# Kernel optimization log

Measured on AMD Instinct MI355X. Metric: run time of the kernel, lower is better.

Reference implementation:

```python
import jax, jax.numpy as jnp
import numpy as np

B, T, C = 2, 2048, 1024
H = 16
D = C // H  # head_size = 64
FF = 4 * C
EPS = 1e-5


def _layernorm(x, g, b):
    mu = jnp.mean(x, axis=-1, keepdims=True)
    var = jnp.var(x, axis=-1, keepdims=True)
    return (x - mu) * jax.lax.rsqrt(var + EPS) * g + b


def setup_inputs() -> dict:
    key = jax.random.key(0)
    ks = jax.random.split(key, 12)
    s_in = 1.0 / np.sqrt(C)
    s_ff = 1.0 / np.sqrt(FF)
    return {
        "x": jax.random.normal(ks[0], (B, T, C), jnp.float32),
        "Wq": jax.random.uniform(ks[1], (H, C, D), jnp.float32, -s_in, s_in),
        "Wk": jax.random.uniform(ks[2], (H, C, D), jnp.float32, -s_in, s_in),
        "Wv": jax.random.uniform(ks[3], (H, C, D), jnp.float32, -s_in, s_in),
        "Wo": jax.random.uniform(ks[4], (C, C), jnp.float32, -s_in, s_in),
        "bo": jax.random.uniform(ks[5], (C,), jnp.float32, -s_in, s_in),
        "W1": jax.random.uniform(ks[6], (C, FF), jnp.float32, -s_in, s_in),
        "b1": jax.random.uniform(ks[7], (FF,), jnp.float32, -s_in, s_in),
        "W2": jax.random.uniform(ks[8], (FF, C), jnp.float32, -s_ff, s_ff),
        "b2": jax.random.uniform(ks[9], (C,), jnp.float32, -s_ff, s_ff),
        "g1": jnp.ones((C,), jnp.float32),
        "be1": jnp.zeros((C,), jnp.float32),
        "g2": jnp.ones((C,), jnp.float32),
        "be2": jnp.zeros((C,), jnp.float32),
    }


def reference(x, Wq, Wk, Wv, Wo, bo, W1, b1, W2, b2, g1, be1, g2, be2):
    h = _layernorm(x, g1, be1)
    # per-head projections (no bias), vectorized over heads
    q = jnp.einsum("btc,hcd->bhtd", h, Wq)
    k = jnp.einsum("btc,hcd->bhtd", h, Wk)
    v = jnp.einsum("btc,hcd->bhtd", h, Wv)
    # NOTE: original scales by n_embd**-0.5 (C, not head_size) -- faithful
    scores = jnp.einsum("bhtd,bhsd->bhts", q, k) * (C ** -0.5)
    causal = jnp.tril(jnp.ones((T, T), bool))
    scores = jnp.where(causal, scores, -jnp.inf)
    att = jax.nn.softmax(scores, axis=-1)
    out = jnp.einsum("bhts,bhsd->bhtd", att, v)
    out = out.transpose(0, 2, 1, 3).reshape(B, T, C)  # concat heads
    x = out @ Wo + bo + x  # attn residual (dropout=0 -> identity)
    h2 = _layernorm(x, g2, be2)
    ff = jax.nn.relu(h2 @ W1 + b1) @ W2 + b2
    return x + ff
```

## Files before the change

### kernel.cpp

```cpp
#include <hip/hip_runtime.h>
#include <stdint.h>

typedef unsigned short ushort_t;
typedef __attribute__((ext_vector_type(8))) short bf16x8;
typedef __attribute__((ext_vector_type(4))) float f32x4;

__device__ __forceinline__ unsigned short f2b(float f) {
  unsigned u = __float_as_uint(f);
  u += 0x7fffu + ((u >> 16) & 1u);
  return (unsigned short)(u >> 16);
}

__device__ __forceinline__ void async16(const void* g, void* l) {
  __builtin_amdgcn_global_load_lds(
      (const __attribute__((address_space(1))) void*)g,
      (__attribute__((address_space(3))) void*)l, 16, 0, 0);
}

__global__ __launch_bounds__(256) void ln_kernel(
    const float* __restrict__ x, const float* __restrict__ g,
    const float* __restrict__ be, ushort_t* __restrict__ out) {
  const int C = 1024;
  int row = blockIdx.x;
  const float4* xr = (const float4*)(x + (size_t)row * C);
  int tid = threadIdx.x;
  float4 v = xr[tid];
  float s = v.x + v.y + v.z + v.w;
  float sq = v.x * v.x + v.y * v.y + v.z * v.z + v.w * v.w;
  #pragma unroll
  for (int off = 32; off > 0; off >>= 1) {
    s += __shfl_xor(s, off);
    sq += __shfl_xor(sq, off);
  }
  __shared__ float ss[4], ssq[4];
  int wv = tid >> 6;
  if ((tid & 63) == 0) { ss[wv] = s; ssq[wv] = sq; }
  __syncthreads();
  s = ss[0] + ss[1] + ss[2] + ss[3];
  sq = ssq[0] + ssq[1] + ssq[2] + ssq[3];
  float mu = s * (1.f / C);
  float var = sq * (1.f / C) - mu * mu;
  float rs = rsqrtf(var + 1e-5f);
  float4 gv = ((const float4*)g)[tid];
  float4 bv = ((const float4*)be)[tid];
  ushort4 o;
  o.x = f2b((v.x - mu) * rs * gv.x + bv.x);
  o.y = f2b((v.y - mu) * rs * gv.y + bv.y);
  o.z = f2b((v.z - mu) * rs * gv.z + bv.z);
  o.w = f2b((v.w - mu) * rs * gv.w + bv.w);
  ((ushort4*)(out + (size_t)row * C))[tid] = o;
}

__global__ __launch_bounds__(256) void reduce2_kernel(
    const float* __restrict__ p0, const float* __restrict__ p1,
    const float* __restrict__ bias, const float* __restrict__ resid,
    float* __restrict__ out) {
  int idx = blockIdx.x * 256 + threadIdx.x;
  float4 a = ((const float4*)p0)[idx];
  float4 b = ((const float4*)p1)[idx];
  float4 r = ((const float4*)resid)[idx];
  float4 bi = ((const float4*)bias)[idx & 255];
  float4 o;
  o.x = a.x + b.x + r.x + bi.x;
  o.y = a.y + b.y + r.y + bi.y;
  o.z = a.z + b.z + r.z + bi.z;
  o.w = a.w + b.w + r.w + bi.w;
  ((float4*)out)[idx] = o;
}

__global__ __launch_bounds__(256) void transpose_all_kernel(
    const float* __restrict__ Wq, const float* __restrict__ Wk,
    const float* __restrict__ Wv, const float* __restrict__ Wo,
    const float* __restrict__ W1, const float* __restrict__ W2,
    ushort_t* __restrict__ qkvt, ushort_t* __restrict__ wot,
    ushort_t* __restrict__ w1t, ushort_t* __restrict__ w2t) {
  int bid = blockIdx.x;
  const float* in;
  ushort_t* out;
  int R, Cin, bx, by;
  if (bid < 3072) {
    int z = bid >> 6, rem = bid & 63;
    bx = rem & 1; by = rem >> 1;
    int wsel = z >> 4, h = z & 15;
    in = (wsel == 0 ? Wq : wsel == 1 ? Wk : Wv) + (size_t)h * 1024 * 64;
    out = qkvt + (size_t)wsel * 1024 * 1024 + (size_t)h * 1024 * 64;
    R = 1024; Cin = 64;
  } else if (bid < 4096) {
    int rem = bid - 3072;
    bx = rem & 31; by = rem >> 5;
    in = Wo; out = wot; R = 1024; Cin = 1024;
  } else if (bid < 8192) {
    int rem = bid - 4096;
    bx = rem & 127; by = rem >> 7;
    in = W1; out = w1t; R = 1024; Cin = 4096;
  } else {
    int rem = bid - 8192;
    bx = rem & 31; by = rem >> 5;
    in = W2; out = w2t; R = 4096; Cin = 1024;
  }
  __shared__ float tile[32][33];
  int c0 = bx * 32, r0 = by * 32;
  int tx = threadIdx.x, ty = threadIdx.y;
  #pragma unroll
  for (int i = 0; i < 4; i++)
    tile[ty + 8 * i][tx] = in[(size_t)(r0 + ty + 8 * i) * Cin + c0 + tx];
  __syncthreads();
  #pragma unroll
  for (int i = 0; i < 4; i++)
    out[(size_t)(c0 + ty + 8 * i) * R + r0 + tx] = f2b(tile[tx][ty + 8 * i]);
}

__global__ __launch_bounds__(256) void transpose_v_kernel(
    const ushort_t* __restrict__ qkv, ushort_t* __restrict__ vt) {
  __shared__ ushort_t tile[32][33];
  int bh = blockIdx.z;
  int b = bh >> 4, h = bh & 15;
  int d0 = blockIdx.x * 32, t0 = blockIdx.y * 32;
  int tx = threadIdx.x, ty = threadIdx.y;
  #pragma unroll
  for (int i = 0; i < 4; i++)
    tile[ty + 8 * i][tx] =
        qkv[(size_t)(b * 2048 + t0 + ty + 8 * i) * 3072 + 2048 + h * 64 + d0 + tx];
  __syncthreads();
  #pragma unroll
  for (int i = 0; i < 4; i++)
    vt[(size_t)(bh * 64 + d0 + ty + 8 * i) * 2048 + t0 + tx] = tile[tx][ty + 8 * i];
}

#define RD_A(DB, MB) \
  _Pragma("unroll") \
  for (int mf_ = 0; mf_ < 4; mf_++) { \
    af[(MB) + mf_][0] = *(const bf16x8*)&Als[DB][wm][(aRow + ((MB) + mf_) * 16) * 64 + rof0]; \
    af[(MB) + mf_][1] = *(const bf16x8*)&Als[DB][wm][(aRow + ((MB) + mf_) * 16) * 64 + rof1]; \
  }
#define RD_B(DB, NB) \
  _Pragma("unroll") \
  for (int nf_ = 0; nf_ < 2; nf_++) { \
    bf[(NB) + nf_][0] = *(const bf16x8*)&Bls[DB][bh][(bRow + ((NB) + nf_) * 16) * 64 + rof0]; \
    bf[(NB) + nf_][1] = *(const bf16x8*)&Bls[DB][bh][(bRow + ((NB) + nf_) * 16) * 64 + rof1]; \
  }
#define MMPH(MB, NB) \
  __builtin_amdgcn_s_barrier(); \
  asm volatile("s_waitcnt lgkmcnt(0)" ::: "memory"); \
  __builtin_amdgcn_sched_barrier(0); \
  __builtin_amdgcn_s_setprio(1); \
  _Pragma("unroll") \
  for (int mf_ = 0; mf_ < 4; mf_++) \
    _Pragma("unroll") \
    for (int nf_ = 0; nf_ < 2; nf_++) { \
      acc[(MB) + mf_][(NB) + nf_] = __builtin_amdgcn_mfma_f32_16x16x32_bf16( \
          af[(MB) + mf_][0], bf[(NB) + nf_][0], acc[(MB) + mf_][(NB) + nf_], 0, 0, 0); \
      acc[(MB) + mf_][(NB) + nf_] = __builtin_amdgcn_mfma_f32_16x16x32_bf16( \
          af[(MB) + mf_][1], bf[(NB) + nf_][1], acc[(MB) + mf_][(NB) + nf_], 0, 0, 0); \
    } \
  __builtin_amdgcn_s_setprio(0);
#define ENDPH __builtin_amdgcn_s_barrier();

template <int N, int K, int FLAGS>
__global__ __launch_bounds__(512, 2) void gemm256p8_kernel(
    const ushort_t* __restrict__ A, const ushort_t* __restrict__ Bt,
    const float* __restrict__ bias, void* __restrict__ outv) {
  constexpr int NBN = N / 256;
  constexpr int NT2 = K / 128;
  __shared__ __align__(16) ushort_t Als[2][2][128 * 64];
  __shared__ __align__(16) ushort_t Bls[2][2][128 * 64];
  int tid = threadIdx.x, w = tid >> 6, lane = tid & 63;
  int quad = lane >> 4, l16 = lane & 15;
  int wm = w >> 2, wn = w & 3;
  int bid = blockIdx.x;
  int bm = bid / NBN, bn = bid % NBN;
  int bm0 = bm * 256, bn0 = bn * 256;
  int lrow = (w << 3) + (lane >> 3);
  int kc8 = ((lane & 7) ^ ((lane >> 3) & 7)) << 3;
  const ushort_t* Ab = A + (size_t)(bm0 + lrow) * K + kc8;
  const ushort_t* Bb = Bt + (size_t)(bn0 + lrow) * K + kc8;
  int rof0 = (quad ^ (l16 & 7)) << 3;
  int rof1 = ((4 + quad) ^ (l16 & 7)) << 3;
  int bh = wn >> 1;
  int aRow = l16;
  int bRow = (wn & 1) * 64 + l16;

  auto stA = [&](int kt, int half, int db) {
    const ushort_t* g = Ab + (size_t)(half * 128) * K + kt * 64;
    ushort_t* l = &Als[db][half][w * 512];
    async16(g, l);
    async16(g + (size_t)64 * K, l + 4096);
  };
  auto stB = [&](int kt, int half, int db) {
    const ushort_t* g = Bb + (size_t)(half * 128) * K + kt * 64;
    ushort_t* l = &Bls[db][half][w * 512];
    async16(g, l);
    async16(g + (size_t)64 * K, l + 4096);
  };

  f32x4 acc[8][4];
  #pragma unroll
  for (int mf = 0; mf < 8; mf++)
    #pragma unroll
    for (int nf = 0; nf < 4; nf++) acc[mf][nf] = f32x4{0.f, 0.f, 0.f, 0.f};
  bf16x8 af[8][2], bf[4][2];

  stA(0, 0, 0); stA(0, 1, 0);
  stB(0, 0, 0); stB(0, 1, 0);
  stA(1, 0, 1); stA(1, 1, 1);
  asm volatile("s_waitcnt vmcnt(4)" ::: "memory");
  __builtin_amdgcn_s_barrier();

  #pragma unroll 1
  for (int i = 0; i < NT2; ++i) {
    bool lastI = (i == NT2 - 1);
    int t1 = 2 * i + 1;
    RD_A(0, 0)
    RD_B(0, 0)
    stB(t1, 0, 1);
    MMPH(0, 0)
    ENDPH
    RD_A(0, 4)
    stB(t1, 1, 1);
    MMPH(4, 0)
    ENDPH
    RD_B(0, 2)
    if (!lastI) stA(t1 + 1, 0, 0);
    MMPH(4, 2)
    ENDPH
    if (!lastI) stA(t1 + 1, 1, 0);
    MMPH(0, 2)
    if (!lastI) asm volatile("s_waitcnt vmcnt(4)" ::: "memory");
    else        asm volatile("s_waitcnt vmcnt(0)" ::: "memory");
    ENDPH
    RD_A(1, 0)
    RD_B(1, 0)
    if (!lastI) stB(t1 + 1, 0, 0);
    MMPH(0, 0)
    ENDPH
    RD_A(1, 4)
    if (!lastI) stB(t1 + 1, 1, 0);
    MMPH(4, 0)
    ENDPH
    RD_B(1, 2)
    if (!lastI) stA(t1 + 2, 0, 1);
    MMPH(4, 2)
    ENDPH
    if (!lastI) stA(t1 + 2, 1, 1);
    MMPH(0, 2)
    if (!lastI) asm volatile("s_waitcnt vmcnt(4)" ::: "memory");
    ENDPH
  }
  #pragma unroll
  for (int mf = 0; mf < 8; mf++)
    #pragma unroll
    for (int nf = 0; nf < 4; nf++)
      #pragma unroll
      for (int r = 0; r < 4; r++) {
        int row = bm0 + wm * 128 + mf * 16 + quad * 4 + r;
        int col = bn0 + wn * 64 + nf * 16 + l16;
        float v = acc[mf][nf][r];
        if constexpr (FLAGS & 4) v += bias[col];
        if constexpr (FLAGS & 1) v = fmaxf(v, 0.f);
        if constexpr ((FLAGS & 2) != 0)
          ((ushort_t*)outv)[(size_t)row * N + col] = f2b(v);
        else
          ((float*)outv)[(size_t)row * N + col] = v;
      }
}
#undef RD_A
#undef RD_B
#undef MMPH
#undef ENDPH

template <int N, int K, int FLAGS, int SK>
__global__ __launch_bounds__(256, 3) void gemm_bt64_kernel(
    const ushort_t* __restrict__ A, const ushort_t* __restrict__ Bt,
    const float* __restrict__ bias, const float* __restrict__ resid,
    void* __restrict__ outv, float* __restrict__ pp0, float* __restrict__ pp1) {
  constexpr int KS = K / SK;
  constexpr int NBM = 32;
  constexpr int NBN = N / 64;
  constexpr int NWG = NBM * NBN * SK;
  __shared__ ushort_t Als[2][128 * 32];
  __shared__ ushort_t Bls[2][64 * 32];
  int tid = threadIdx.x, w = tid >> 6, lane = tid & 63, quad = lane >> 4, l16 = lane & 15;
  int bid = blockIdx.x;
  int swz = (bid & 7) * (NWG / 8) + (bid >> 3);
  int z = 0;
  if constexpr (SK > 1) { z = swz / (NBM * NBN); swz -= z * (NBM * NBN); }
  int bm = swz / NBN, bn = swz - bm * NBN;
  int bm0 = bm * 128, bn0 = bn * 64;
  int koff = z * KS;
  int wm = (w >> 1) * 64, wn = (w & 1) * 32;
  f32x4 acc[4][2];
  #pragma unroll
  for (int i = 0; i < 4; i++)
    #pragma unroll
    for (int j = 0; j < 2; j++) acc[i][j] = f32x4{0.f, 0.f, 0.f, 0.f};
  const ushort_t* Ag = A + (size_t)bm0 * K + koff;
  const ushort_t* Bg = Bt + (size_t)bn0 * K + koff;
  int lr = lane >> 2, lco = (lane & 3) * 8;
  auto stage = [&](int k0, int bi) {
    async16(Ag + (size_t)(w * 32 + lr) * K + k0 + lco, &Als[bi][w * 1024]);
    async16(Ag + (size_t)(w * 32 + 16 + lr) * K + k0 + lco, &Als[bi][w * 1024 + 512]);
    async16(Bg + (size_t)(w * 16 + lr) * K + k0 + lco, &Bls[bi][w * 512]);
  };
  stage(0, 0);
  int s = 0;
  for (int k0 = 0; k0 < KS; k0 += 32, s ^= 1) {
    __syncthreads();
    if (k0 + 32 < KS) stage(k0 + 32, s ^ 1);
    bf16x8 af[4], bf[2];
    #pragma unroll
    for (int i = 0; i < 4; i++)
      af[i] = *(const bf16x8*)&Als[s][(wm + i * 16 + l16) * 32 + quad * 8];
    #pragma unroll
    for (int j = 0; j < 2; j++)
      bf[j] = *(const bf16x8*)&Bls[s][(wn + j * 16 + l16) * 32 + quad * 8];
    #pragma unroll
    for (int i = 0; i < 4; i++)
      #pragma unroll
      for (int j = 0; j < 2; j++)
        acc[i][j] = __builtin_amdgcn_mfma_f32_16x16x32_bf16(af[i], bf[j], acc[i][j], 0, 0, 0);
  }
  float* pdst = nullptr;
  if constexpr (SK > 1) pdst = z ? pp1 : pp0;
  #pragma unroll
  for (int i = 0; i < 4; i++)
    #pragma unroll
    for (int j = 0; j < 2; j++)
      #pragma unroll
      for (int r = 0; r < 4; r++) {
        int row = bm0 + wm + i * 16 + quad * 4 + r;
        int col = bn0 + wn + j * 16 + l16;
        float v = acc[i][j][r];
        if constexpr (SK > 1) {
          pdst[(size_t)row * N + col] = v;
        } else {
          if constexpr (FLAGS & 4) v += bias[col];
          if constexpr (FLAGS & 8) v += resid[(size_t)row * N + col];
          if constexpr (FLAGS & 1) v = fmaxf(v, 0.f);
          if constexpr ((FLAGS & 2) != 0)
            ((ushort_t*)outv)[(size_t)row * N + col] = f2b(v);
          else
            ((float*)outv)[(size_t)row * N + col] = v;
        }
      }
}

__global__ __launch_bounds__(256, 4) void attn_kernel(
    const ushort_t* __restrict__ qkv, const ushort_t* __restrict__ vt,
    ushort_t* __restrict__ out) {
  const int T = 2048, CC = 3072;
  __shared__ ushort_t Kls[2][2 * 64 * 32];
  __shared__ ushort_t Vls[2][2 * 64 * 32];
  int fid = blockIdx.x;
  int bh = (fid & 7) * 4 + ((fid >> 3) & 3);
  int qb = 31 - (fid >> 5);
  int b = bh >> 4, h = bh & 15;
  int q0 = qb * 64;
  int tid = threadIdx.x, w = tid >> 6, lane = tid & 63, quad = lane >> 4, l16 = lane & 15;
  int srow = w * 16 + (lane >> 2);
  int sco = (lane & 3) * 8;
  const ushort_t* kg = qkv + (size_t)(b * T + srow) * CC + 1024 + h * 64 + sco;
  const ushort_t* vg = vt + (size_t)(bh * 64 + srow) * T + sco;
  int q0s = q0 + w * 16;
  int trow = q0s + l16;
  const ushort_t* qp = qkv + (size_t)(b * T + trow) * CC + h * 64 + quad * 8;
  bf16x8 aq[2] = { *(const bf16x8*)qp, *(const bf16x8*)(qp + 32) };
  f32x4 O[4];
  #pragma unroll
  for (int i = 0; i < 4; i++) O[i] = f32x4{0.f, 0.f, 0.f, 0.f};
  float mrun = -1e30f, lrun = 0.f;
  const float ksc = 0.03125f * 1.44269504f;
  int src0 = (quad & 1) * 32 + l16;
  int src1 = src0 + 16;
  bool hiq = quad >= 2;
  auto stage = [&](int kb, int bi) {
    int s0 = kb * 64;
    async16(kg + (size_t)s0 * CC, &Kls[bi][w * 512]);
    async16(kg + (size_t)s0 * CC + 32, &Kls[bi][2048 + w * 512]);
    async16(vg + s0, &Vls[bi][w * 512]);
    async16(vg + s0 + 32, &Vls[bi][2048 + w * 512]);
  };
  stage(0, 0);
  for (int kb = 0; kb <= qb; kb++) {
    __syncthreads();
    if (kb < qb) stage(kb + 1, (kb + 1) & 1);
    int bi = kb & 1;
    int s0 = kb * 64;
    bf16x8 kfr[4][2], vfr[4][2];
    #pragma unroll
    for (int t = 0; t < 4; t++)
      #pragma unroll
      for (int ks = 0; ks < 2; ks++) {
        kfr[t][ks] = *(const bf16x8*)&Kls[bi][(ks * 64 + t * 16 + l16) * 32 + quad * 8];
        vfr[t][ks] = *(const bf16x8*)&Vls[bi][(ks * 64 + t * 16 + l16) * 32 + quad * 8];
      }
    f32x4 st[4];
    #pragma unroll
    for (int t = 0; t < 4; t++) {
      st[t] = f32x4{0.f, 0.f, 0.f, 0.f};
      #pragma unroll
      for (int ks = 0; ks < 2; ks++)
        st[t] = __builtin_amdgcn_mfma_f32_16x16x32_bf16(kfr[t][ks], aq[ks], st[t], 0, 0, 0);
    }
    float sv[4][4];
    float vmax = -1e30f;
    if (kb == qb) {
      #pragma unroll
      for (int t = 0; t < 4; t++)
        #pragma unroll
        for (int r = 0; r < 4; r++) {
          float sc = st[t][r] * ksc;
          int scol = s0 + t * 16 + quad * 4 + r;
          if (scol > trow) sc = -1e30f;
          sv[t][r] = sc;
          vmax = fmaxf(vmax, sc);
        }
    } else {
      #pragma unroll
      for (int t = 0; t < 4; t++)
        #pragma unroll
        for (int r = 0; r < 4; r++) {
          float sc = st[t][r] * ksc;
          sv[t][r] = sc;
          vmax = fmaxf(vmax, sc);
        }
    }
    vmax = fmaxf(vmax, __shfl_xor(vmax, 16));
    vmax = fmaxf(vmax, __shfl_xor(vmax, 32));
    float mnew = fmaxf(mrun, vmax);
    float alpha = __builtin_amdgcn_exp2f(mrun - mnew);
    mrun = mnew;
    float psum = 0.f;
    int pk[4][2];
    #pragma unroll
    for (int t = 0; t < 4; t++) {
      float p0 = __builtin_amdgcn_exp2f(sv[t][0] - mnew);
      float p1 = __builtin_amdgcn_exp2f(sv[t][1] - mnew);
      float p2 = __builtin_amdgcn_exp2f(sv[t][2] - mnew);
      float p3 = __builtin_amdgcn_exp2f(sv[t][3] - mnew);
      psum += (p0 + p1) + (p2 + p3);
      pk[t][0] = (int)((unsigned)f2b(p0) | ((unsigned)f2b(p1) << 16));
      pk[t][1] = (int)((unsigned)f2b(p2) | ((unsigned)f2b(p3) << 16));
    }
    psum += __shfl_xor(psum, 16);
    psum += __shfl_xor(psum, 32);
    lrun = lrun * alpha + psum;
    #pragma unroll
    for (int dt = 0; dt < 4; dt++) O[dt] *= alpha;
    #pragma unroll
    for (int g32 = 0; g32 < 2; g32++) {
      int t0 = 2 * g32, t1 = t0 + 1;
      int a0 = __shfl(pk[t0][0], src0), b0 = __shfl(pk[t1][0], src0);
      int a1 = __shfl(pk[t0][1], src0), b1 = __shfl(pk[t1][1], src0);
      int a2 = __shfl(pk[t0][0], src1), b2 = __shfl(pk[t1][0], src1);
      int a3 = __shfl(pk[t0][1], src1), b3 = __shfl(pk[t1][1], src1);
      union { int4 i; bf16x8 h; } u;
      u.i.x = hiq ? b0 : a0;
      u.i.y = hiq ? b1 : a1;
      u.i.z = hiq ? b2 : a2;
      u.i.w = hiq ? b3 : a3;
      #pragma unroll
      for (int dt = 0; dt < 4; dt++)
        O[dt] = __builtin_amdgcn_mfma_f32_16x16x32_bf16(vfr[dt][g32], u.h, O[dt], 0, 0, 0);
    }
  }
  float inv = 1.f / lrun;
  #pragma unroll
  for (int dt = 0; dt < 4; dt++) {
    ushort4 o;
    unsigned short* op = (unsigned short*)&o;
    #pragma unroll
    for (int r = 0; r < 4; r++) op[r] = f2b(O[dt][r] * inv);
    *(ushort4*)&out[(size_t)(b * T + trow) * 1024 + h * 64 + dt * 16 + quad * 4] = o;
  }
}

extern "C" void kernel_launch(void* const* d_in, const int* in_sizes, int n_in,
                              void* d_out, int out_size, void* d_ws, size_t ws_size,
                              hipStream_t stream) {
  const int B = 2, T = 2048, C = 1024, H = 16, D = 64, FF = 4096;
  const int M = B * T;
  const float* x   = (const float*)d_in[0];
  const float* Wq  = (const float*)d_in[1];
  const float* Wk  = (const float*)d_in[2];
  const float* Wv  = (const float*)d_in[3];
  const float* Wo  = (const float*)d_in[4];
  const float* bo  = (const float*)d_in[5];
  const float* W1  = (const float*)d_in[6];
  const float* b1  = (const float*)d_in[7];
  const float* W2  = (const float*)d_in[8];
  const float* b2  = (const float*)d_in[9];
  const float* g1  = (const float*)d_in[10];
  const float* be1 = (const float*)d_in[11];
  const float* g2  = (const float*)d_in[12];
  const float* be2 = (const float*)d_in[13];
  float* out = (float*)d_out;

  char* ws = (char*)d_ws;
  size_t off = 0;
  auto alloc = [&](size_t bytes) {
    void* p = ws + off;
    off += (bytes + 255) & ~(size_t)255;
    return p;
  };
  ushort_t* qkvt = (ushort_t*)alloc((size_t)3 * C * C * 2);
  ushort_t* wot  = (ushort_t*)alloc((size_t)C * C * 2);
  ushort_t* w1t  = (ushort_t*)alloc((size_t)FF * C * 2);
  ushort_t* w2t  = (ushort_t*)alloc((size_t)C * FF * 2);
  ushort_t* hbuf = (ushort_t*)alloc((size_t)M * C * 2);
  ushort_t* big  = (ushort_t*)alloc((size_t)M * FF * 2);
  ushort_t* vtb  = (ushort_t*)alloc((size_t)M * C * 2);
  ushort_t* aout = (ushort_t*)alloc((size_t)M * C * 2);
  float*    x2   = (float*)alloc((size_t)M * C * 4);
  float* pf0 = (float*)vtb;
  float* pf1 = (float*)qkvt;

  dim3 tb(32, 8);
  transpose_all_kernel<<<12288, tb, 0, stream>>>(
      Wq, Wk, Wv, Wo, W1, W2, qkvt, wot, w1t, w2t);
  ln_kernel<<<M, 256, 0, stream>>>(x, g1, be1, hbuf);
  gemm256p8_kernel<3072, 1024, 2><<<192, 512, 0, stream>>>(
      hbuf, qkvt, nullptr, big);
  transpose_v_kernel<<<dim3(2, T / 32, B * H), tb, 0, stream>>>(big, vtb);
  attn_kernel<<<1024, 256, 0, stream>>>(big, vtb, aout);
  gemm_bt64_kernel<1024, 1024, 4 | 8, 1><<<512, 256, 0, stream>>>(
      aout, wot, bo, x, x2, nullptr, nullptr);
  ln_kernel<<<M, 256, 0, stream>>>(x2, g2, be2, hbuf);
  gemm256p8_kernel<4096, 1024, 1 | 2 | 4><<<256, 512, 0, stream>>>(
      hbuf, w1t, b1, big);
  gemm_bt64_kernel<1024, 4096, 0, 2><<<1024, 256, 0, stream>>>(
      big, w2t, nullptr, nullptr, nullptr, pf0, pf1);
  reduce2_kernel<<<M * C / 1024, 256, 0, stream>>>(pf0, pf1, b2, x2, out);
}
```

Measured before the change: 355.7 us.

## Run FFN down-projection on 256x256 GEMM kernel with 4-way split-K

The W2 down-projection (K=4096, N=1024) moves from the 64-wide bt64 GEMM with 2-way split-K to the larger 256x256 eight-wave GEMM, using 4-way split-K so the grid has 256 workgroups. The four partial sums go to scratch buffers, with the fourth written straight into the output, and a three-input reduce kernel adds them with bias and residual. hbuf is enlarged so it can hold a float partial. The larger tile raises data reuse per workgroup, at the cost of more partial-sum traffic to global memory.

```diff
diff --git a/kernel.cpp b/kernel.cpp
--- a/kernel.cpp
+++ b/kernel.cpp
@@ -51,20 +51,21 @@
   ((ushort4*)(out + (size_t)row * C))[tid] = o;
 }
 
-__global__ __launch_bounds__(256) void reduce2_kernel(
+__global__ __launch_bounds__(256) void reduce3_kernel(
     const float* __restrict__ p0, const float* __restrict__ p1,
-    const float* __restrict__ bias, const float* __restrict__ resid,
-    float* __restrict__ out) {
+    const float* __restrict__ p2, const float* __restrict__ bias,
+    const float* __restrict__ resid, float* out) {
   int idx = blockIdx.x * 256 + threadIdx.x;
   float4 a = ((const float4*)p0)[idx];
   float4 b = ((const float4*)p1)[idx];
+  float4 c = ((const float4*)p2)[idx];
   float4 r = ((const float4*)resid)[idx];
   float4 bi = ((const float4*)bias)[idx & 255];
-  float4 o;
-  o.x = a.x + b.x + r.x + bi.x;
-  o.y = a.y + b.y + r.y + bi.y;
-  o.z = a.z + b.z + r.z + bi.z;
-  o.w = a.w + b.w + r.w + bi.w;
+  float4 o = ((const float4*)out)[idx];
+  o.x += a.x + b.x + c.x + r.x + bi.x;
+  o.y += a.y + b.y + c.y + r.y + bi.y;
+  o.z += a.z + b.z + c.z + r.z + bi.z;
+  o.w += a.w + b.w + c.w + r.w + bi.w;
   ((float4*)out)[idx] = o;
 }
 
@@ -136,8 +137,8 @@
 #define RD_B(DB, NB) \
   _Pragma("unroll") \
   for (int nf_ = 0; nf_ < 2; nf_++) { \
-    bf[(NB) + nf_][0] = *(const bf16x8*)&Bls[DB][bh][(bRow + ((NB) + nf_) * 16) * 64 + rof0]; \
-    bf[(NB) + nf_][1] = *(const bf16x8*)&Bls[DB][bh][(bRow + ((NB) + nf_) * 16) * 64 + rof1]; \
+    bf[(NB) + nf_][0] = *(const bf16x8*)&Bls[DB][bhh][(bRow + ((NB) + nf_) * 16) * 64 + rof0]; \
+    bf[(NB) + nf_][1] = *(const bf16x8*)&Bls[DB][bhh][(bRow + ((NB) + nf_) * 16) * 64 + rof1]; \
   }
 #define MMPH(MB, NB) \
   __builtin_amdgcn_s_barrier(); \
@@ -156,27 +157,34 @@
   __builtin_amdgcn_s_setprio(0);
 #define ENDPH __builtin_amdgcn_s_barrier();
 
-template <int N, int K, int FLAGS>
+template <int N, int K, int FLAGS, int SK>
 __global__ __launch_bounds__(512, 2) void gemm256p8_kernel(
     const ushort_t* __restrict__ A, const ushort_t* __restrict__ Bt,
-    const float* __restrict__ bias, void* __restrict__ outv) {
+    const float* __restrict__ bias, void* __restrict__ outv,
+    float* __restrict__ pp0, float* __restrict__ pp1,
+    float* __restrict__ pp2, float* __restrict__ pp3) {
+  constexpr int NBM = 4096 / 256;
   constexpr int NBN = N / 256;
-  constexpr int NT2 = K / 128;
+  constexpr int KS = K / SK;
+  constexpr int NT2 = KS / 128;
   __shared__ __align__(16) ushort_t Als[2][2][128 * 64];
   __shared__ __align__(16) ushort_t Bls[2][2][128 * 64];
   int tid = threadIdx.x, w = tid >> 6, lane = tid & 63;
   int quad = lane >> 4, l16 = lane & 15;
   int wm = w >> 2, wn = w & 3;
   int bid = blockIdx.x;
-  int bm = bid / NBN, bn = bid % NBN;
+  int z = 0, rem = bid;
+  if constexpr (SK > 1) { z = bid / (NBM * NBN); rem = bid - z * (NBM * NBN); }
+  int bm = rem / NBN, bn = rem % NBN;
   int bm0 = bm * 256, bn0 = bn * 256;
+  int koff = z * KS;
   int lrow = (w << 3) + (lane >> 3);
   int kc8 = ((lane & 7) ^ ((lane >> 3) & 7)) << 3;
-  const ushort_t* Ab = A + (size_t)(bm0 + lrow) * K + kc8;
-  const ushort_t* Bb = Bt + (size_t)(bn0 + lrow) * K + kc8;
+  const ushort_t* Ab = A + (size_t)(bm0 + lrow) * K + koff + kc8;
+  const ushort_t* Bb = Bt + (size_t)(bn0 + lrow) * K + koff + kc8;
   int rof0 = (quad ^ (l16 & 7)) << 3;
   int rof1 = ((4 + quad) ^ (l16 & 7)) << 3;
-  int bh = wn >> 1;
+  int bhh = wn >> 1;
   int aRow = l16;
   int bRow = (wn & 1) * 64 + l16;
 
@@ -246,22 +254,36 @@
     if (!lastI) asm volatile("s_waitcnt vmcnt(4)" ::: "memory");
     ENDPH
   }
-  #pragma unroll
-  for (int mf = 0; mf < 8; mf++)
-    #pragma unroll
-    for (int nf = 0; nf < 4; nf++)
-      #pragma unroll
-      for (int r = 0; r < 4; r++) {
-        int row = bm0 + wm * 128 + mf * 16 + quad * 4 + r;
-        int col = bn0 + wn * 64 + nf * 16 + l16;
-        float v = acc[mf][nf][r];
-        if constexpr (FLAGS & 4) v += bias[col];
-        if constexpr (FLAGS & 1) v = fmaxf(v, 0.f);
-        if constexpr ((FLAGS & 2) != 0)
-          ((ushort_t*)outv)[(size_t)row * N + col] = f2b(v);
-        else
-          ((float*)outv)[(size_t)row * N + col] = v;
-      }
+  if constexpr (SK > 1) {
+    float* pdst = z == 0 ? pp0 : z == 1 ? pp1 : z == 2 ? pp2 : pp3;
+    #pragma unroll
+    for (int mf = 0; mf < 8; mf++)
+      #pragma unroll
+      for (int nf = 0; nf < 4; nf++)
+        #pragma unroll
+        for (int r = 0; r < 4; r++) {
+          int row = bm0 + wm * 128 + mf * 16 + quad * 4 + r;
+          int col = bn0 + wn * 64 + nf * 16 + l16;
+          pdst[(size_t)row * N + col] = acc[mf][nf][r];
+        }
+  } else {
+    #pragma unroll
+    for (int mf = 0; mf < 8; mf++)
+      #pragma unroll
+      for (int nf = 0; nf < 4; nf++)
+        #pragma unroll
+        for (int r = 0; r < 4; r++) {
+          int row = bm0 + wm * 128 + mf * 16 + quad * 4 + r;
+          int col = bn0 + wn * 64 + nf * 16 + l16;
+          float v = acc[mf][nf][r];
+          if constexpr (FLAGS & 4) v += bias[col];
+          if constexpr (FLAGS & 1) v = fmaxf(v, 0.f);
+          if constexpr ((FLAGS & 2) != 0)
+            ((ushort_t*)outv)[(size_t)row * N + col] = f2b(v);
+          else
+            ((float*)outv)[(size_t)row * N + col] = v;
+        }
+  }
 }
 #undef RD_A
 #undef RD_B
@@ -506,28 +528,29 @@
   ushort_t* wot  = (ushort_t*)alloc((size_t)C * C * 2);
   ushort_t* w1t  = (ushort_t*)alloc((size_t)FF * C * 2);
   ushort_t* w2t  = (ushort_t*)alloc((size_t)C * FF * 2);
-  ushort_t* hbuf = (ushort_t*)alloc((size_t)M * C * 2);
+  ushort_t* hbuf = (ushort_t*)alloc((size_t)M * C * 4);
   ushort_t* big  = (ushort_t*)alloc((size_t)M * FF * 2);
   ushort_t* vtb  = (ushort_t*)alloc((size_t)M * C * 2);
   ushort_t* aout = (ushort_t*)alloc((size_t)M * C * 2);
   float*    x2   = (float*)alloc((size_t)M * C * 4);
-  float* pf0 = (float*)vtb;
-  float* pf1 = (float*)qkvt;
+  float* pf0 = (float*)qkvt;
+  float* pf1 = (float*)hbuf;
+  float* pf2 = (float*)vtb;
 
   dim3 tb(32, 8);
   transpose_all_kernel<<<12288, tb, 0, stream>>>(
       Wq, Wk, Wv, Wo, W1, W2, qkvt, wot, w1t, w2t);
   ln_kernel<<<M, 256, 0, stream>>>(x, g1, be1, hbuf);
-  gemm256p8_kernel<3072, 1024, 2><<<192, 512, 0, stream>>>(
-      hbuf, qkvt, nullptr, big);
+  gemm256p8_kernel<3072, 1024, 2, 1><<<192, 512, 0, stream>>>(
+      hbuf, qkvt, nullptr, big, nullptr, nullptr, nullptr, nullptr);
   transpose_v_kernel<<<dim3(2, T / 32, B * H), tb, 0, stream>>>(big, vtb);
   attn_kernel<<<1024, 256, 0, stream>>>(big, vtb, aout);
   gemm_bt64_kernel<1024, 1024, 4 | 8, 1><<<512, 256, 0, stream>>>(
       aout, wot, bo, x, x2, nullptr, nullptr);
   ln_kernel<<<M, 256, 0, stream>>>(x2, g2, be2, hbuf);
-  gemm256p8_kernel<4096, 1024, 1 | 2 | 4><<<256, 512, 0, stream>>>(
-      hbuf, w1t, b1, big);
-  gemm_bt64_kernel<1024, 4096, 0, 2><<<1024, 256, 0, stream>>>(
-      big, w2t, nullptr, nullptr, nullptr, pf0, pf1);
-  reduce2_kernel<<<M * C / 1024, 256, 0, stream>>>(pf0, pf1, b2, x2, out);
-}
+  gemm256p8_kernel<4096, 1024, 1 | 2 | 4, 1><<<256, 512, 0, stream>>>(
+      hbuf, w1t, b1, big, nullptr, nullptr, nullptr, nullptr);
+  gemm256p8_kernel<1024, 4096, 0, 4><<<256, 512, 0, stream>>>(
+      big, w2t, nullptr, nullptr, pf0, pf1, pf2, out);
+  reduce3_kernel<<<M * C / 1024, 256, 0, stream>>>(pf0, pf1, pf2, b2, x2, out);
+}
```

New measurement: 351.2 us. About the same (-1.3%).
